# Optimization experiments

Measured on AMD Instinct MI355X. Metric: run time of the kernel, lower is better.

## Reference

```python
import jax, jax.numpy as jnp
import numpy as np

S, O, H = 8, 1024, 1024
B, N = 32, 512

def setup_inputs() -> dict:
    key = jax.random.key(0)
    k1, k2, k3, k4 = jax.random.split(key, 4)
    x = jax.random.normal(k1, (B, N, H), dtype=jnp.float32)
    subject_id = jax.random.randint(k2, (B,), 0, S)
    # kaiming_uniform_(a=sqrt(5)) on [S,O,H]: fan_in=H, gain=sqrt(2/(1+5)), bound=gain*sqrt(3/fan_in)
    wbound = jnp.sqrt(2.0 / 6.0) * jnp.sqrt(3.0 / H)
    weight = jax.random.uniform(k3, (S, O, H), minval=-wbound, maxval=wbound, dtype=jnp.float32)
    bbound = 1.0 / jnp.sqrt(H)
    bias = jax.random.uniform(k4, (S, O), minval=-bbound, maxval=bbound, dtype=jnp.float32)
    return {"x": x, "subject_id": subject_id, "weight": weight, "bias": bias}

def reference(x, subject_id, weight, bias):
    # Per-sample weight gather + batched matmul + bias add
    W = weight[subject_id]          # [B, O, H]
    b = bias[subject_id]            # [B, O]
    y = jnp.einsum('bnh,boh->bno', x, W) + b[:, None, :]
    return y
```

## Files before the change

kernel.cpp:

```cpp
#include <hip/hip_runtime.h>


constexpr int S_DIM = 8;
constexpr int O_DIM = 1024;
constexpr int H_DIM = 1024;
constexpr int B_DIM = 32;
constexpr int N_DIM = 512;

constexpr int BM = 128;
constexpr int BN = 128;
constexpr int BK = 64;
constexpr int NTHREADS = 256;

constexpr long long X_ELEMS = (long long)B_DIM * N_DIM * H_DIM;
constexpr long long W_ELEMS = (long long)S_DIM * O_DIM * H_DIM;
constexpr size_t XB_BYTES = (size_t)X_ELEMS * 2;

typedef short bf16x8 __attribute__((ext_vector_type(8)));
typedef float f32x4 __attribute__((ext_vector_type(4)));
typedef float f32x2 __attribute__((ext_vector_type(2)));
typedef __bf16 bf16x2 __attribute__((ext_vector_type(2)));

__device__ __forceinline__ unsigned int cvt_pk_bf16(float a, float b) {
  f32x2 v;
  v[0] = a;
  v[1] = b;
  bf16x2 r = __builtin_convertvector(v, bf16x2);
  return __builtin_bit_cast(unsigned int, r);
}

__device__ __forceinline__ void gload_lds16(const void* g, void* l) {
  __builtin_amdgcn_global_load_lds(
      (const __attribute__((address_space(1))) unsigned int*)g,
      (__attribute__((address_space(3))) unsigned int*)l, 16, 0, 0);
}

__global__ __launch_bounds__(256) void cvt_kernel(
    const float* __restrict__ x, const float* __restrict__ w,
    unsigned short* __restrict__ xb, unsigned short* __restrict__ wb) {
  const long long t = (long long)blockIdx.x * 256 + threadIdx.x;
  const long long XT = X_ELEMS / 8;
  const float* src;
  unsigned short* dst;
  long long i;
  if (t < XT) {
    src = x; dst = xb; i = t;
  } else {
    src = w; dst = wb; i = t - XT;
  }
  const f32x4* p = (const f32x4*)(src + i * 8);
  const f32x4 a = p[0];
  const f32x4 c = p[1];
  uint4 u;
  u.x = cvt_pk_bf16(a[0], a[1]);
  u.y = cvt_pk_bf16(a[2], a[3]);
  u.z = cvt_pk_bf16(c[0], c[1]);
  u.w = cvt_pk_bf16(c[2], c[3]);
  *(uint4*)(dst + i * 8) = u;
}

__global__ __launch_bounds__(NTHREADS, 4) void scl_gemm(
    const unsigned short* __restrict__ xb, const int* __restrict__ subject_id,
    const unsigned short* __restrict__ wb, const float* __restrict__ bias,
    float* __restrict__ out) {
  __shared__ __align__(16) unsigned short As[BM * BK];
  __shared__ __align__(16) unsigned short Bs[BN * BK];

  const int tid = threadIdx.x;
  const int b = blockIdx.z;
  const int n0 = blockIdx.x * BM;
  const int o0 = blockIdx.y * BN;
  const int sid = subject_id[b];

  const int lane = tid & 63;
  const int wid = tid >> 6;
  const int wm0 = (wid >> 1) * 64;
  const int wn0 = (wid & 1) * 64;
  const int lcol = lane & 15;
  const int lq = lane >> 4;

  const int srow = wid * 32 + (lane >> 3);
  const int skc = (lane & 7) * 8;
  const unsigned short* ag = xb + (size_t)(b * N_DIM + n0 + srow) * H_DIM + skc;
  const unsigned short* bg = wb + (size_t)(sid * O_DIM + o0 + srow) * H_DIM + skc;
  unsigned short* as_base = &As[(wid * 32) * BK];
  unsigned short* bs_base = &Bs[(wid * 32) * BK];

  f32x4 acc[4][4];
#pragma unroll
  for (int mi = 0; mi < 4; ++mi)
#pragma unroll
    for (int ni = 0; ni < 4; ++ni) {
      f32x4 z = {0.f, 0.f, 0.f, 0.f};
      acc[mi][ni] = z;
    }

  for (int k0 = 0; k0 < H_DIM; k0 += BK) {
    __syncthreads();
#pragma unroll
    for (int i = 0; i < 4; ++i) {
      gload_lds16(ag + (size_t)(i * 8) * H_DIM + k0, as_base + i * 8 * BK);
      gload_lds16(bg + (size_t)(i * 8) * H_DIM + k0, bs_base + i * 8 * BK);
    }
    __syncthreads();

#pragma unroll
    for (int kk = 0; kk < BK; kk += 32) {
      const int kb = kk + lq * 8;
      bf16x8 af[4], bfr[4];
#pragma unroll
      for (int mi = 0; mi < 4; ++mi)
        af[mi] = *(const bf16x8*)(&As[(wm0 + mi * 16 + lcol) * BK + kb]);
#pragma unroll
      for (int ni = 0; ni < 4; ++ni)
        bfr[ni] = *(const bf16x8*)(&Bs[(wn0 + ni * 16 + lcol) * BK + kb]);
#pragma unroll
      for (int mi = 0; mi < 4; ++mi)
#pragma unroll
        for (int ni = 0; ni < 4; ++ni)
          acc[mi][ni] = __builtin_amdgcn_mfma_f32_16x16x32_bf16(
              af[mi], bfr[ni], acc[mi][ni], 0, 0, 0);
    }
  }

  float bv[4];
#pragma unroll
  for (int ni = 0; ni < 4; ++ni)
    bv[ni] = bias[sid * O_DIM + o0 + wn0 + ni * 16 + lcol];

  float* outb = out + (size_t)(b * N_DIM + n0 + wm0) * O_DIM + o0 + wn0 + lcol;
#pragma unroll
  for (int mi = 0; mi < 4; ++mi) {
#pragma unroll
    for (int r = 0; r < 4; ++r) {
      float* orow = outb + (size_t)(mi * 16 + lq * 4 + r) * O_DIM;
#pragma unroll
      for (int ni = 0; ni < 4; ++ni)
        orow[ni * 16] = acc[mi][ni][r] + bv[ni];
    }
  }
}

extern "C" void kernel_launch(void* const* d_in, const int* in_sizes, int n_in,
                              void* d_out, int out_size, void* d_ws, size_t ws_size,
                              hipStream_t stream) {
  const float* x = (const float*)d_in[0];
  const int* subject_id = (const int*)d_in[1];
  const float* weight = (const float*)d_in[2];
  const float* bias = (const float*)d_in[3];
  float* out = (float*)d_out;

  unsigned short* xb = (unsigned short*)d_ws;
  unsigned short* wb = (unsigned short*)((char*)d_ws + XB_BYTES);

  const long long cvt_threads = (X_ELEMS + W_ELEMS) / 8;
  cvt_kernel<<<(int)(cvt_threads / 256), 256, 0, stream>>>(x, weight, xb, wb);

  dim3 grid(N_DIM / BM, O_DIM / BN, B_DIM);
  scl_gemm<<<grid, NTHREADS, 0, stream>>>(xb, subject_id, wb, bias, out);
}
```

Before: 188.8 us.

## XOR-swizzle LDS tiles and restructure fp32-to-bf16 conversion kernel

The GEMM now writes each 16-byte chunk of the A and B tiles into shared memory at a column chunk index XORed with the row's low bits, and the fragment reads apply the same XOR. This is meant to remove LDS bank conflicts on the row-strided bf16x8 reads. The conversion kernel now has each block handle a 4096-element chunk, with per-thread float4 nontemporal loads over four coalesced strides and the x/weight split made per block. The nontemporal hint may keep converted inputs out of cache before the GEMM reads them.

```diff
diff --git a/kernel.cpp b/kernel.cpp
--- a/kernel.cpp
+++ b/kernel.cpp
@@ -38,25 +38,24 @@
 __global__ __launch_bounds__(256) void cvt_kernel(
     const float* __restrict__ x, const float* __restrict__ w,
     unsigned short* __restrict__ xb, unsigned short* __restrict__ wb) {
-  const long long t = (long long)blockIdx.x * 256 + threadIdx.x;
-  const long long XT = X_ELEMS / 8;
+  const int blk = blockIdx.x;
   const float* src;
   unsigned short* dst;
-  long long i;
-  if (t < XT) {
-    src = x; dst = xb; i = t;
+  long long base;
+  if (blk < 4096) {
+    src = x; dst = xb; base = (long long)blk * 4096;
   } else {
-    src = w; dst = wb; i = t - XT;
+    src = w; dst = wb; base = (long long)(blk - 4096) * 4096;
   }
-  const f32x4* p = (const f32x4*)(src + i * 8);
-  const f32x4 a = p[0];
-  const f32x4 c = p[1];
-  uint4 u;
-  u.x = cvt_pk_bf16(a[0], a[1]);
-  u.y = cvt_pk_bf16(a[2], a[3]);
-  u.z = cvt_pk_bf16(c[0], c[1]);
-  u.w = cvt_pk_bf16(c[2], c[3]);
-  *(uint4*)(dst + i * 8) = u;
+  const long long e0 = base + threadIdx.x * 4;
+#pragma unroll
+  for (int c = 0; c < 4; ++c) {
+    const f32x4 v = __builtin_nontemporal_load((const f32x4*)(src + e0 + c * 1024));
+    uint2 u;
+    u.x = cvt_pk_bf16(v[0], v[1]);
+    u.y = cvt_pk_bf16(v[2], v[3]);
+    *(uint2*)(dst + e0 + c * 1024) = u;
+  }
 }
 
 __global__ __launch_bounds__(NTHREADS, 4) void scl_gemm(
@@ -79,8 +78,9 @@
   const int lcol = lane & 15;
   const int lq = lane >> 4;
 
-  const int srow = wid * 32 + (lane >> 3);
-  const int skc = (lane & 7) * 8;
+  const int rl = lane >> 3;
+  const int srow = wid * 32 + rl;
+  const int skc = ((lane & 7) ^ rl) * 8;
   const unsigned short* ag = xb + (size_t)(b * N_DIM + n0 + srow) * H_DIM + skc;
   const unsigned short* bg = wb + (size_t)(sid * O_DIM + o0 + srow) * H_DIM + skc;
   unsigned short* as_base = &As[(wid * 32) * BK];
@@ -106,14 +106,18 @@
 
 #pragma unroll
     for (int kk = 0; kk < BK; kk += 32) {
-      const int kb = kk + lq * 8;
+      const int clog = (kk >> 3) + lq;
       bf16x8 af[4], bfr[4];
 #pragma unroll
-      for (int mi = 0; mi < 4; ++mi)
-        af[mi] = *(const bf16x8*)(&As[(wm0 + mi * 16 + lcol) * BK + kb]);
+      for (int mi = 0; mi < 4; ++mi) {
+        const int ar = wm0 + mi * 16 + lcol;
+        af[mi] = *(const bf16x8*)(&As[ar * BK + ((clog ^ (ar & 7)) << 3)]);
+      }
 #pragma unroll
-      for (int ni = 0; ni < 4; ++ni)
-        bfr[ni] = *(const bf16x8*)(&Bs[(wn0 + ni * 16 + lcol) * BK + kb]);
+      for (int ni = 0; ni < 4; ++ni) {
+        const int br = wn0 + ni * 16 + lcol;
+        bfr[ni] = *(const bf16x8*)(&Bs[br * BK + ((clog ^ (br & 7)) << 3)]);
+      }
 #pragma unroll
       for (int mi = 0; mi < 4; ++mi)
 #pragma unroll
@@ -153,8 +157,7 @@
   unsigned short* xb = (unsigned short*)d_ws;
   unsigned short* wb = (unsigned short*)((char*)d_ws + XB_BYTES);
 
-  const long long cvt_threads = (X_ELEMS + W_ELEMS) / 8;
-  cvt_kernel<<<(int)(cvt_threads / 256), 256, 0, stream>>>(x, weight, xb, wb);
+  cvt_kernel<<<6144, 256, 0, stream>>>(x, weight, xb, wb);
 
   dim3 grid(N_DIM / BM, O_DIM / BN, B_DIM);
   scl_gemm<<<grid, NTHREADS, 0, stream>>>(xb, subject_id, wb, bias, out);
```

Measured after the change: 180.3 us. 1.05x faster.
